# Optimization experiments

Hardware: AMD Instinct MI355X
Metric: run time of the kernel (lower is better)

The kernel has to match this reference:

```python
import jax, jax.numpy as jnp
import numpy as np

B, S, DIN, DOUT = 4, 2048, 4096, 4096

def setup_inputs() -> dict:
    key = jax.random.key(0)
    k1, k2, k3, k4 = jax.random.split(key, 4)
    x = jax.random.normal(k1, (B, S, DIN), dtype=jnp.float32)
    # symmetric int8 weight values in [-127, 127]
    quantized_weight = jax.random.randint(k2, (DOUT, DIN), -127, 128, dtype=jnp.int32).astype(jnp.int8)
    weight_scale = jax.random.uniform(k3, (), dtype=jnp.float32) * 0.01 + 1e-4
    bias = jax.random.normal(k4, (DOUT,), dtype=jnp.float32)
    return {"x": x, "quantized_weight": quantized_weight, "weight_scale": weight_scale, "bias": bias}

def reference(x, quantized_weight, weight_scale, bias) -> jnp.ndarray:
    # dequantize_tensor: (q.float() - 0) * scale
    weight_fp32 = quantized_weight.astype(jnp.float32) * weight_scale  # [DOUT, DIN]
    # nn.functional.linear: x @ W^T + b
    return jnp.einsum('bsi,oi->bso', x, weight_fp32) + bias
```

## Files before the change

kernel.cpp:

```cpp
#include <hip/hip_runtime.h>
#include <stdint.h>
#include <stddef.h>

constexpr int MDIM = 8192;
constexpr int NDIM = 4096;
constexpr int KDIM = 4096;

using f32x4 = __attribute__((ext_vector_type(4))) float;
using s16x4 = __attribute__((ext_vector_type(4))) short;
using s16x8 = __attribute__((ext_vector_type(8))) short;
using i32x4 = __attribute__((ext_vector_type(4))) int;

__device__ __forceinline__ short f32_to_bf16_rn(float f) {
  union { float f; uint32_t u; } v; v.f = f;
  uint32_t r = (v.u + 0x7FFFu + ((v.u >> 16) & 1u)) >> 16;
  return (short)(uint16_t)r;
}

__global__ void __launch_bounds__(256) quant_x_kernel(const float* __restrict__ in,
                                                      signed char* __restrict__ out,
                                                      float* __restrict__ sx) {
  const int row = blockIdx.x;
  const int t   = threadIdx.x;
  const float* rp = in + (size_t)row * KDIM;
  f32x4 v[4];
  float m = 0.0f;
#pragma unroll
  for (int j = 0; j < 4; ++j) {
    v[j] = *(const f32x4*)(rp + t * 16 + j * 4);
#pragma unroll
    for (int e = 0; e < 4; ++e) m = fmaxf(m, __builtin_fabsf(v[j][e]));
  }
#pragma unroll
  for (int off = 32; off > 0; off >>= 1) m = fmaxf(m, __shfl_xor(m, off, 64));
  __shared__ float wmax[4];
  const int wv = t >> 6, ln = t & 63;
  if (ln == 0) wmax[wv] = m;
  __syncthreads();
  m = fmaxf(fmaxf(wmax[0], wmax[1]), fmaxf(wmax[2], wmax[3]));
  const float inv = (m > 0.0f) ? (127.0f / m) : 0.0f;
  if (t == 0) sx[row] = m * (1.0f / 127.0f);
  i32x4 o;
#pragma unroll
  for (int j = 0; j < 4; ++j) {
    int b[4];
#pragma unroll
    for (int e = 0; e < 4; ++e) {
      int q = (int)rintf(v[j][e] * inv);
      q = q < -127 ? -127 : (q > 127 ? 127 : q);
      b[e] = q & 255;
    }
    o[j] = b[0] | (b[1] << 8) | (b[2] << 16) | (b[3] << 24);
  }
  *(i32x4*)(out + (size_t)row * KDIM + t * 16) = o;
}

__global__ void __launch_bounds__(256) quant_w_kernel(const int* __restrict__ in,
                                                      signed char* __restrict__ out, int n16) {
  int i = blockIdx.x * 256 + threadIdx.x;
  const int stride = gridDim.x * 256;
  for (; i < n16; i += stride) {
    const i32x4* p = (const i32x4*)(in + (size_t)i * 16);
    i32x4 o;
#pragma unroll
    for (int j = 0; j < 4; ++j) {
      i32x4 a = p[j];
      o[j] = (a[0] & 255) | ((a[1] & 255) << 8) | ((a[2] & 255) << 16) | ((a[3] & 255) << 24);
    }
    *(i32x4*)(out + (size_t)i * 16) = o;
  }
}


#define BAR asm volatile("s_barrier" ::: "memory")
#define WAITVM(n) asm volatile("s_waitcnt vmcnt(" #n ")" ::: "memory")

#define GLL(src, dst) __builtin_amdgcn_global_load_lds(                     \
    (const __attribute__((address_space(1))) void*)(src),                   \
    (__attribute__((address_space(3))) void*)(dst), 16, 0, 0)

#define STG(grow, ldsmat, tau) do {                                         \
  const int buf_ = (tau) & 1;                                               \
  GLL((grow) + (size_t)r0 * 4096 + (size_t)(tau) * 64 + cb,                 \
      lds + (ldsmat) + buf_ * 16384 + t * 16);                              \
  GLL((grow) + (size_t)r1 * 4096 + (size_t)(tau) * 64 + cb,                 \
      lds + (ldsmat) + buf_ * 16384 + 8192 + t * 16);                       \
} while (0)

#define LDA8(bufc, i) (*(const i32x4*)(lds + (bufc) * 16384                 \
    + (wm * 8 + (i)) * 1024 + laneoff))
#define LDB8(bufc, j) (*(const i32x4*)(lds + 32768 + (bufc) * 16384         \
    + (wn * 4 + (j)) * 1024 + laneoff))

#define MFMAQ(base, afr, bset) do {                                         \
  __builtin_amdgcn_s_setprio(1);                                            \
  _Pragma("unroll") for (int i_ = 0; i_ < 4; ++i_)                          \
  _Pragma("unroll") for (int j_ = 0; j_ < 4; ++j_)                          \
    acc[(base) + i_][j_] = __builtin_amdgcn_mfma_i32_16x16x64_i8(           \
        afr[i_], bfr[bset][j_], acc[(base) + i_][j_], 0, 0, 0);             \
  __builtin_amdgcn_s_setprio(0);                                            \
} while (0)

#define KT8(t_, cur, nxt, s1, s2, r1x, r2x, vm1, vm2) do {                  \
                                                                    \
  _Pragma("unroll") for (int i_ = 0; i_ < 4; ++i_) afhi[i_] = LDA8(cur, 4 + i_); \
  if (r1x) { _Pragma("unroll") for (int j_ = 0; j_ < 4; ++j_)               \
    bfr[nxt][j_] = LDB8(nxt, j_); }                                         \
  if (s1) STG(Brow, 32768, (t_) + 2);                                       \
  MFMAQ(0, aflo, cur);                                                      \
  if ((vm1) == 2) { WAITVM(2); } else if ((vm1) == 0) { WAITVM(0); }        \
  BAR;                                                                      \
                                                                    \
  if (r2x) { _Pragma("unroll") for (int i_ = 0; i_ < 4; ++i_)               \
    aflo[i_] = LDA8(nxt, i_); }                                             \
  if (s2) STG(Arow, 0, (t_) + 2);                                           \
  MFMAQ(4, afhi, cur);                                                      \
  if ((vm2) == 2) { WAITVM(2); } else if ((vm2) == 0) { WAITVM(0); }        \
  BAR;                                                                      \
} while (0)

__global__ void __launch_bounds__(512, 2) gemm_i8_pipe(
    const signed char* __restrict__ A, const signed char* __restrict__ Bw,
    const float* __restrict__ sx, const float* __restrict__ scale_p,
    const float* __restrict__ bias, float* __restrict__ out) {
  __shared__ __align__(16) char lds[65536];

  const int t      = threadIdx.x;
  const int lane   = t & 63;
  const int wave   = t >> 6;
  const int wm     = wave >> 2;
  const int wn     = wave & 3;
  const int lane15 = lane & 15;
  const int lh     = lane >> 4;

  const int laneoff = (lane15 * 64 + lh * 16) ^ ((lane15 & 8) << 2);

  const int ax = ((t >> 5) & 1) << 5;
  const int a0 = (t * 16) ^ ax;
  const int a1 = (8192 + t * 16) ^ ax;
  const int r0 = a0 >> 6;
  const int r1 = a1 >> 6;
  const int cb = a0 & 63;

  const int bid   = blockIdx.x;
  const int wg    = (bid & 7) * 64 + (bid >> 3);
  const int ntile = wg & 15;
  const int mtile = wg >> 4;
  const int m0 = mtile * 256;
  const int n0 = ntile * 256;

  const char* Arow = (const char*)(A + (size_t)m0 * KDIM);
  const char* Brow = (const char*)(Bw + (size_t)n0 * KDIM);

  i32x4 acc[8][4] = {};
  i32x4 aflo[4], afhi[4], bfr[2][4];

  STG(Brow, 32768, 0);
  STG(Arow, 0,     0);
  STG(Brow, 32768, 1);
  STG(Arow, 0,     1);
  WAITVM(2);
  BAR;
#pragma unroll
  for (int i_ = 0; i_ < 4; ++i_) aflo[i_] = LDA8(0, i_);
#pragma unroll
  for (int j_ = 0; j_ < 4; ++j_) bfr[0][j_] = LDB8(0, j_);

#pragma unroll 1
  for (int tp = 0; tp < 31; ++tp) {
    KT8(2 * tp,     0, 1, 1, 1, 1, 1, 2, 2);
    KT8(2 * tp + 1, 1, 0, 1, 1, 1, 1, 2, 2);
  }
  KT8(62, 0, 1, 0, 0, 1, 1, 0, -1);
  KT8(63, 1, 0, 0, 0, 0, 0, -1, -1);

  const float sw = scale_p[0];
  float bv[4];
#pragma unroll
  for (int j = 0; j < 4; ++j) bv[j] = bias[n0 + wn * 64 + j * 16 + lane15];
#pragma unroll
  for (int i = 0; i < 8; ++i) {
    const int rowb = m0 + wm * 128 + i * 16 + lh * 4;
    float sxq[4];
#pragma unroll
    for (int q = 0; q < 4; ++q) sxq[q] = sx[rowb + q] * sw;
#pragma unroll
    for (int j = 0; j < 4; ++j) {
      const int col = n0 + wn * 64 + j * 16 + lane15;
#pragma unroll
      for (int q = 0; q < 4; ++q)
        out[(size_t)(rowb + q) * NDIM + col] = (float)acc[i][j][q] * sxq[q] + bv[j];
    }
  }
}

constexpr int FTILE = 128;
constexpr int FBK   = 64;

__global__ void __launch_bounds__(256) gemm_raw(
    const float* __restrict__ X, const int* __restrict__ W,
    const float* __restrict__ scale_p, const float* __restrict__ bias,
    float* __restrict__ out) {
  __shared__ short As[FTILE * FBK];
  __shared__ short Bs[FTILE * FBK];

  const int t      = threadIdx.x;
  const int lane   = t & 63;
  const int wave   = t >> 6;
  const int wm     = wave >> 1;
  const int wn     = wave & 1;
  const int lane15   = lane & 15;
  const int laneHalf = lane >> 4;

  const int bid   = blockIdx.x;
  const int wg    = (bid & 7) * 256 + (bid >> 3);
  const int ntile = wg & 31;
  const int mtile = wg >> 5;
  const int m0 = mtile * FTILE;
  const int n0 = ntile * FTILE;

  f32x4 acc[4][4] = {};

  for (int k0 = 0; k0 < KDIM; k0 += FBK) {
    __syncthreads();
#pragma unroll
    for (int r = 0; r < 8; ++r) {
      const int f   = r * 256 + t;
      const int row = f >> 4;
      const int c4  = (f & 15) * 4;
      f32x4 v = *(const f32x4*)(X + (size_t)(m0 + row) * KDIM + (k0 + c4));
      s16x4 h;
#pragma unroll
      for (int j = 0; j < 4; ++j) h[j] = f32_to_bf16_rn(v[j]);
      *(s16x4*)&As[row * FBK + c4] = h;

      i32x4 wv = *(const i32x4*)(W + (size_t)(n0 + row) * KDIM + (k0 + c4));
      s16x4 hw;
#pragma unroll
      for (int j = 0; j < 4; ++j) hw[j] = f32_to_bf16_rn((float)wv[j]);
      *(s16x4*)&Bs[row * FBK + c4] = hw;
    }
    __syncthreads();

#pragma unroll
    for (int kk = 0; kk < FBK; kk += 32) {
      const int kb = kk + laneHalf * 8;
      s16x8 af[4], bf[4];
#pragma unroll
      for (int i = 0; i < 4; ++i) {
        af[i] = *(const s16x8*)&As[(wm * 64 + i * 16 + lane15) * FBK + kb];
        bf[i] = *(const s16x8*)&Bs[(wn * 64 + i * 16 + lane15) * FBK + kb];
      }
#pragma unroll
      for (int i = 0; i < 4; ++i)
#pragma unroll
        for (int j = 0; j < 4; ++j)
          acc[i][j] = __builtin_amdgcn_mfma_f32_16x16x32_bf16(af[i], bf[j], acc[i][j], 0, 0, 0);
    }
  }

  const float s = scale_p[0];
#pragma unroll
  for (int j = 0; j < 4; ++j) {
    const int col = n0 + wn * 64 + j * 16 + lane15;
    const float bv = bias[col];
#pragma unroll
    for (int i = 0; i < 4; ++i) {
      const int row = m0 + wm * 64 + i * 16 + laneHalf * 4;
#pragma unroll
      for (int q = 0; q < 4; ++q)
        out[(size_t)(row + q) * NDIM + col] = acc[i][j][q] * s + bv;
    }
  }
}

extern "C" void kernel_launch(void* const* d_in, const int* in_sizes, int n_in,
                              void* d_out, int out_size, void* d_ws, size_t ws_size,
                              hipStream_t stream) {
  const float* x     = (const float*)d_in[0];
  const int*   w     = (const int*)d_in[1];
  const float* scale = (const float*)d_in[2];
  const float* bias  = (const float*)d_in[3];
  float* out = (float*)d_out;

  const size_t a_bytes = (size_t)MDIM * KDIM;
  const size_t b_bytes = (size_t)NDIM * KDIM;
  const size_t need    = a_bytes + b_bytes + MDIM * 4;

  if (ws_size >= need) {
    signed char* Ai8 = (signed char*)d_ws;
    signed char* Bi8 = Ai8 + a_bytes;
    float*       sxp = (float*)(Bi8 + b_bytes);
    quant_x_kernel<<<MDIM, 256, 0, stream>>>(x, Ai8, sxp);
    quant_w_kernel<<<4096, 256, 0, stream>>>(w, Bi8, (int)(b_bytes / 16));
    const int nwg = (MDIM / 256) * (NDIM / 256);
    gemm_i8_pipe<<<nwg, 512, 0, stream>>>(Ai8, Bi8, sxp, scale, bias, out);
  } else {
    const int nwg = (MDIM / FTILE) * (NDIM / FTILE);
    gemm_raw<<<nwg, 256, 0, stream>>>(x, w, scale, bias, out);
  }
}
```

Measured before the change: 184.4 us.

## Double the K tile to 128 and restructure the LDS pipeline into four MFMA phases

Each staged K tile grows from 64 to 128 bytes, split into two 64-wide halves, and the shared-memory buffers double to 128 KB. The main loop is rebuilt so each tile runs four MFMA phases separated by barriers. The next tile is staged one step ahead and is waited for at the end of each tile. The previous scheme prefetched fragments into registers across phases. The aim is to halve the number of loop iterations and global-load waits. The cost is more barriers, no register-level prefetch overlap, and an LDS footprint that likely prevents two blocks from sharing a CU despite the launch bounds.

```diff
diff --git a/kernel.cpp b/kernel.cpp
--- a/kernel.cpp
+++ b/kernel.cpp
@@ -79,43 +79,47 @@
     (const __attribute__((address_space(1))) void*)(src),                   \
     (__attribute__((address_space(3))) void*)(dst), 16, 0, 0)
 
-#define STG(grow, ldsmat, tau) do {                                         \
+#define STG4(grow, ldsmat, tau) do {                                        \
   const int buf_ = (tau) & 1;                                               \
-  GLL((grow) + (size_t)r0 * 4096 + (size_t)(tau) * 64 + cb,                 \
-      lds + (ldsmat) + buf_ * 16384 + t * 16);                              \
-  GLL((grow) + (size_t)r1 * 4096 + (size_t)(tau) * 64 + cb,                 \
-      lds + (ldsmat) + buf_ * 16384 + 8192 + t * 16);                       \
+  _Pragma("unroll") for (int h_ = 0; h_ < 2; ++h_)                          \
+  _Pragma("unroll") for (int rh_ = 0; rh_ < 2; ++rh_)                       \
+    GLL((grow) + (size_t)(rh_ * 128 + r0) * 4096 + (size_t)(tau) * 128      \
+            + h_ * 64 + cb,                                                 \
+        lds + (ldsmat) + buf_ * 32768 + h_ * 16384 + rh_ * 8192 + t * 16);  \
 } while (0)
 
-#define LDA8(bufc, i) (*(const i32x4*)(lds + (bufc) * 16384                 \
-    + (wm * 8 + (i)) * 1024 + laneoff))
-#define LDB8(bufc, j) (*(const i32x4*)(lds + 32768 + (bufc) * 16384         \
-    + (wn * 4 + (j)) * 1024 + laneoff))
-
-#define MFMAQ(base, afr, bset) do {                                         \
+#define LDA8(bufc, fi, h) (*(const i32x4*)(lds + (bufc) * 32768             \
+    + (h) * 16384 + wmoff + (fi) * 1024 + laneoff))
+#define LDB8(bufc, fj, h) (*(const i32x4*)(lds + 65536 + (bufc) * 32768     \
+    + (h) * 16384 + wnoff + (fj) * 1024 + laneoff))
+
+#define MFMAQ(base, afr) do {                                               \
   __builtin_amdgcn_s_setprio(1);                                            \
   _Pragma("unroll") for (int i_ = 0; i_ < 4; ++i_)                          \
   _Pragma("unroll") for (int j_ = 0; j_ < 4; ++j_)                          \
     acc[(base) + i_][j_] = __builtin_amdgcn_mfma_i32_16x16x64_i8(           \
-        afr[i_], bfr[bset][j_], acc[(base) + i_][j_], 0, 0, 0);             \
+        afr[i_], bf[j_], acc[(base) + i_][j_], 0, 0, 0);                    \
   __builtin_amdgcn_s_setprio(0);                                            \
 } while (0)
 
-#define KT8(t_, cur, nxt, s1, s2, r1x, r2x, vm1, vm2) do {                  \
-                                                                    \
-  _Pragma("unroll") for (int i_ = 0; i_ < 4; ++i_) afhi[i_] = LDA8(cur, 4 + i_); \
-  if (r1x) { _Pragma("unroll") for (int j_ = 0; j_ < 4; ++j_)               \
-    bfr[nxt][j_] = LDB8(nxt, j_); }                                         \
-  if (s1) STG(Brow, 32768, (t_) + 2);                                       \
-  MFMAQ(0, aflo, cur);                                                      \
-  if ((vm1) == 2) { WAITVM(2); } else if ((vm1) == 0) { WAITVM(0); }        \
-  BAR;                                                                      \
-                                                                    \
-  if (r2x) { _Pragma("unroll") for (int i_ = 0; i_ < 4; ++i_)               \
-    aflo[i_] = LDA8(nxt, i_); }                                             \
-  if (s2) STG(Arow, 0, (t_) + 2);                                           \
-  MFMAQ(4, afhi, cur);                                                      \
-  if ((vm2) == 2) { WAITVM(2); } else if ((vm2) == 0) { WAITVM(0); }        \
+#define KT128(t_, cur, stg) do {                                            \
+                                                   \
+  _Pragma("unroll") for (int j_ = 0; j_ < 4; ++j_) bf[j_] = LDB8(cur, j_, 0); \
+  _Pragma("unroll") for (int i_ = 0; i_ < 4; ++i_) af[i_] = LDA8(cur, i_, 0); \
+  if (stg) STG4(Brow, 65536, (t_) + 1);                                     \
+  BAR; MFMAQ(0, af); BAR;                                                   \
+                                       \
+  _Pragma("unroll") for (int i_ = 0; i_ < 4; ++i_) ag[i_] = LDA8(cur, 4 + i_, 0); \
+  if (stg) STG4(Arow, 0, (t_) + 1);                                         \
+  BAR; MFMAQ(4, ag); BAR;                                                   \
+                                                   \
+  _Pragma("unroll") for (int j_ = 0; j_ < 4; ++j_) bf[j_] = LDB8(cur, j_, 1); \
+  _Pragma("unroll") for (int i_ = 0; i_ < 4; ++i_) af[i_] = LDA8(cur, i_, 1); \
+  BAR; MFMAQ(0, af); BAR;                                                   \
+                                                   \
+  _Pragma("unroll") for (int i_ = 0; i_ < 4; ++i_) ag[i_] = LDA8(cur, 4 + i_, 1); \
+  BAR; MFMAQ(4, ag);                                                        \
+  if (stg) WAITVM(0);                                                       \
   BAR;                                                                      \
 } while (0)
 
@@ -123,7 +127,7 @@
     const signed char* __restrict__ A, const signed char* __restrict__ Bw,
     const float* __restrict__ sx, const float* __restrict__ scale_p,
     const float* __restrict__ bias, float* __restrict__ out) {
-  __shared__ __align__(16) char lds[65536];
+  __shared__ __align__(16) char lds[131072];
 
   const int t      = threadIdx.x;
   const int lane   = t & 63;
@@ -134,12 +138,12 @@
   const int lh     = lane >> 4;
 
   const int laneoff = (lane15 * 64 + lh * 16) ^ ((lane15 & 8) << 2);
+  const int wmoff   = wm * 8192;
+  const int wnoff   = wn * 4096;
 
   const int ax = ((t >> 5) & 1) << 5;
   const int a0 = (t * 16) ^ ax;
-  const int a1 = (8192 + t * 16) ^ ax;
   const int r0 = a0 >> 6;
-  const int r1 = a1 >> 6;
   const int cb = a0 & 63;
 
   const int bid   = blockIdx.x;
@@ -153,26 +157,20 @@
   const char* Brow = (const char*)(Bw + (size_t)n0 * KDIM);
 
   i32x4 acc[8][4] = {};
-  i32x4 aflo[4], afhi[4], bfr[2][4];
-
-  STG(Brow, 32768, 0);
-  STG(Arow, 0,     0);
-  STG(Brow, 32768, 1);
-  STG(Arow, 0,     1);
-  WAITVM(2);
+  i32x4 af[4], ag[4], bf[4];
+
+  STG4(Brow, 65536, 0);
+  STG4(Arow, 0,     0);
+  WAITVM(0);
   BAR;
-#pragma unroll
-  for (int i_ = 0; i_ < 4; ++i_) aflo[i_] = LDA8(0, i_);
-#pragma unroll
-  for (int j_ = 0; j_ < 4; ++j_) bfr[0][j_] = LDB8(0, j_);
 
 #pragma unroll 1
-  for (int tp = 0; tp < 31; ++tp) {
-    KT8(2 * tp,     0, 1, 1, 1, 1, 1, 2, 2);
-    KT8(2 * tp + 1, 1, 0, 1, 1, 1, 1, 2, 2);
-  }
-  KT8(62, 0, 1, 0, 0, 1, 1, 0, -1);
-  KT8(63, 1, 0, 0, 0, 0, 0, -1, -1);
+  for (int tp = 0; tp < 15; ++tp) {
+    KT128(2 * tp,     0, 1);
+    KT128(2 * tp + 1, 1, 1);
+  }
+  KT128(30, 0, 1);
+  KT128(31, 1, 0);
 
   const float sw = scale_p[0];
   float bv[4];
```

New measurement: 184.9 us. Within noise of the previous version (+0.2%).
